# Optimization experiments

Measured on AMD Instinct MI355X. Metric: run time of the kernel, lower is better.

The kernel has to match this reference:

```python
import jax, jax.numpy as jnp
import numpy as np

B, N, C = 8, 1374, 768
H = 12
HD = C // H  # 64
HIDDEN = int(C * 4.0)  # 3072
EPS = 1e-5


def setup_inputs() -> dict:
    key = jax.random.key(0)
    ks = jax.random.split(key, 12)
    s = 0.02
    return {
        "x": jax.random.normal(ks[0], (B, N, C), jnp.float32),
        "rope_freqs": jax.random.normal(ks[1], (1, N, 1, HD), jnp.float32),
        "ln1_g": jnp.ones((C,), jnp.float32),
        "ln1_b": jnp.zeros((C,), jnp.float32),
        "qkv_w": jax.random.normal(ks[2], (3 * C, C), jnp.float32) * s,
        "qkv_b": jnp.zeros((3 * C,), jnp.float32),
        "proj_w": jax.random.normal(ks[3], (C, C), jnp.float32) * s,
        "proj_b": jnp.zeros((C,), jnp.float32),
        "ln2_g": jnp.ones((C,), jnp.float32),
        "ln2_b": jnp.zeros((C,), jnp.float32),
        "w1": jax.random.normal(ks[4], (HIDDEN, C), jnp.float32) * s,
        "b1": jnp.zeros((HIDDEN,), jnp.float32),
        "w2": jax.random.normal(ks[5], (HIDDEN, C), jnp.float32) * s,
        "b2": jnp.zeros((HIDDEN,), jnp.float32),
        "w3": jax.random.normal(ks[6], (C, HIDDEN), jnp.float32) * s,
        "b3": jnp.zeros((C,), jnp.float32),
    }


def _layernorm(x, g, b):
    mu = jnp.mean(x, axis=-1, keepdims=True)
    var = jnp.mean(jnp.square(x - mu), axis=-1, keepdims=True)
    return (x - mu) * jax.lax.rsqrt(var + EPS) * g + b


def _rotate_half(x):
    x1, x2 = jnp.split(x, 2, axis=-1)
    return jnp.concatenate([-x2, x1], axis=-1)


def _apply_rope(q, k, freqs):
    # freqs: [1, N, 1, HD] -> [1, 1, N, HD] (matches torch permute(0,2,1,3))
    f = jnp.transpose(freqs, (0, 2, 1, 3))
    cos, sin = jnp.cos(f), jnp.sin(f)
    q_rot = q * cos + _rotate_half(q) * sin
    k_rot = k * cos + _rotate_half(k) * sin
    return q_rot, k_rot


def reference(x, rope_freqs, ln1_g, ln1_b, qkv_w, qkv_b, proj_w, proj_b,
              ln2_g, ln2_b, w1, b1, w2, b2, w3, b3):
    scale = HD ** -0.5
    # --- Attention branch ---
    h = _layernorm(x, ln1_g, ln1_b)
    qkv = jnp.einsum('bnc,dc->bnd', h, qkv_w) + qkv_b          # [B,N,3C]
    qkv = qkv.reshape(B, N, 3, H, HD).transpose(2, 0, 3, 1, 4)  # [3,B,H,N,HD]
    q, k, v = qkv[0], qkv[1], qkv[2]
    # rope_freqs covers all N tokens -> n_special = 0 path
    q, k = _apply_rope(q, k, rope_freqs)
    attn = jnp.einsum('bhnd,bhmd->bhnm', q, k) * scale          # [B,H,N,N]
    attn = jax.nn.softmax(attn, axis=-1)
    o = jnp.einsum('bhnm,bhmd->bhnd', attn, v)                  # [B,H,N,HD]
    o = o.transpose(0, 2, 1, 3).reshape(B, N, C)
    o = jnp.einsum('bnc,dc->bnd', o, proj_w) + proj_b
    x = x + o
    # --- SwiGLU MLP branch ---
    h2 = _layernorm(x, ln2_g, ln2_b)
    x1 = jnp.einsum('bnc,hc->bnh', h2, w1) + b1
    x2 = jnp.einsum('bnc,hc->bnh', h2, w2) + b2
    hid = jax.nn.silu(x1) * x2
    mlp_out = jnp.einsum('bnh,ch->bnc', hid, w3) + b3
    return x + mlp_out
```

## Files before the change

kernel.cpp:

```cpp
#include <hip/hip_runtime.h>
#include <stdint.h>

#define B_ 8
#define N_ 1374
#define C_ 768
#define H_ 12
#define HD_ 64
#define HID_ 3072
#define M_ (B_*N_)
#define MPAD_ 11008
#define QT_ 22
#define QT2_ 11

#define QSC_ 0.18033688011112042f

typedef __attribute__((ext_vector_type(8))) short short8;
typedef __attribute__((ext_vector_type(4))) float f32x4;
typedef __attribute__((ext_vector_type(4))) _Float16 half4;
typedef __attribute__((ext_vector_type(2))) _Float16 half2v;

__device__ __forceinline__ unsigned short f2bf(float f) {
  unsigned u = __float_as_uint(f);
  u += 0x7FFF + ((u >> 16) & 1);
  return (unsigned short)(u >> 16);
}
__device__ __forceinline__ float bf2f(unsigned short h) {
  return __uint_as_float(((unsigned)h) << 16);
}
__device__ __forceinline__ unsigned short f2h(float f) {
  return __builtin_bit_cast(unsigned short, (_Float16)f);
}

__device__ __forceinline__ half2v pkrtz(float a, float b) {
  return __builtin_bit_cast(half2v, __builtin_amdgcn_cvt_pkrtz(a, b));
}

#if __has_builtin(__builtin_amdgcn_global_load_lds)
#define HAVE_GLL 1
#endif

__device__ __forceinline__ void gld16(const unsigned short* g, unsigned short* l) {
#ifdef HAVE_GLL
  __builtin_amdgcn_global_load_lds((const __attribute__((address_space(1))) void*)g,
                                   (__attribute__((address_space(3))) void*)l, 16, 0, 0);
#else
  *(short8*)l = *(const short8*)g;
#endif
}

__global__ __launch_bounds__(256) void cvt5_kernel(
    const float* __restrict__ s0, const float* __restrict__ s1,
    const float* __restrict__ s2, const float* __restrict__ s3,
    const float* __restrict__ s4, unsigned short* __restrict__ out) {
  int id = blockIdx.x * 256 + threadIdx.x;
  const float* src; int off;
  if (id < 442368)        { src = s0; off = id; }
  else if (id < 589824)   { src = s1; off = id - 442368; }
  else if (id < 1179648)  { src = s2; off = id - 589824; }
  else if (id < 1769472)  { src = s3; off = id - 1179648; }
  else                    { src = s4; off = id - 1769472; }
  float4 v = ((const float4*)src)[off];
  ushort4 o;
  o.x = f2bf(v.x); o.y = f2bf(v.y); o.z = f2bf(v.z); o.w = f2bf(v.w);
  ((ushort4*)out)[id] = o;
}

__global__ __launch_bounds__(256) void ln_kernel(const float* __restrict__ in,
    const float* __restrict__ g, const float* __restrict__ bta,
    unsigned short* __restrict__ out) {
  int row = blockIdx.x;
  int t = threadIdx.x;
  const float* xr = in + (size_t)row * C_;
  float v0 = xr[t], v1 = xr[t + 256], v2 = xr[t + 512];
  float s1 = v0 + v1 + v2;
  float s2 = v0*v0 + v1*v1 + v2*v2;
  for (int off = 1; off < 64; off <<= 1) {
    s1 += __shfl_xor(s1, off, 64);
    s2 += __shfl_xor(s2, off, 64);
  }
  __shared__ float r1[4], r2[4];
  int wave = t >> 6, lane = t & 63;
  if (lane == 0) { r1[wave] = s1; r2[wave] = s2; }
  __syncthreads();
  float tot1 = r1[0] + r1[1] + r1[2] + r1[3];
  float tot2 = r2[0] + r2[1] + r2[2] + r2[3];
  float mu = tot1 * (1.0f / C_);
  float var = tot2 * (1.0f / C_) - mu * mu;
  float rs = rsqrtf(var + 1e-5f);
  size_t ob = (size_t)row * C_;
  out[ob + t]       = f2bf((v0 - mu) * rs * g[t]       + bta[t]);
  out[ob + t + 256] = f2bf((v1 - mu) * rs * g[t + 256] + bta[t + 256]);
  out[ob + t + 512] = f2bf((v2 - mu) * rs * g[t + 512] + bta[t + 512]);
}

template<int EPI, int ROPE, int TM, int SWZ>
__global__ __launch_bounds__(256, (TM == 64) ? 4 : 2) void gemm_bt(
    const unsigned short* __restrict__ A,
    const unsigned short* __restrict__ W,
    void* __restrict__ outp,
    const float* __restrict__ bias0,
    const float* __restrict__ resid,
    const float* __restrict__ freqs,
    int K, int ldo, int Mvalid, int X)
{
  constexpr int MI = TM / 32;
  __shared__ __align__(16) unsigned short As[2][TM * 32];
  __shared__ __align__(16) unsigned short Bs[2][4096];
  const int t = threadIdx.x;
  const int lane = t & 63;
  const int wave = t >> 6;
  const int wm = (wave >> 1) * (TM / 2);
  const int wn = (wave & 1) * 64;
  const int lr = lane & 15;
  const int lg = lane >> 4;
  const int lk = lg * 8;
  int bx, by;
  if (SWZ) {
    int Y = gridDim.x / X;
    int lin = blockIdx.x;
    int sgsz = X * 8;
    int sg = lin / sgsz;
    int base_y = sg * 8;
    int rows = Y - base_y; if (rows > 8) rows = 8;
    int within = lin - sg * sgsz;
    by = base_y + within % rows;
    bx = within / rows;
  } else {
    bx = blockIdx.x % X;
    by = blockIdx.x / X;
  }
  const int tm0 = by * TM;
  const int tn0 = bx * 128;
  const int r0 = t >> 2;
  const int c0 = (t & 3) * 8;
  const unsigned short* ga0 = A + (size_t)(tm0 + r0) * K + c0;
  const unsigned short* ga1 = A + (size_t)(tm0 + 64 + r0) * K + c0;
  const unsigned short* gb0 = W + (size_t)(tn0 + r0) * K + c0;
  const unsigned short* gb1 = W + (size_t)(tn0 + 64 + r0) * K + c0;
  f32x4 zero = {0.f, 0.f, 0.f, 0.f};
  f32x4 acc[MI][4];
#pragma unroll
  for (int mi = 0; mi < MI; ++mi)
#pragma unroll
    for (int ni = 0; ni < 4; ++ni) acc[mi][ni] = zero;

  for (int kt = 0; kt < K; kt += 64) {
    __syncthreads();
    gld16(ga0 + kt,      &As[0][t * 8]);
    gld16(ga0 + kt + 32, &As[1][t * 8]);
    if (TM == 128) {
      gld16(ga1 + kt,      &As[0][2048 + t * 8]);
      gld16(ga1 + kt + 32, &As[1][2048 + t * 8]);
    }
    gld16(gb0 + kt,      &Bs[0][t * 8]);
    gld16(gb1 + kt,      &Bs[0][2048 + t * 8]);
    gld16(gb0 + kt + 32, &Bs[1][t * 8]);
    gld16(gb1 + kt + 32, &Bs[1][2048 + t * 8]);
    __syncthreads();
#pragma unroll
    for (int u = 0; u < 2; ++u) {
      short8 af[MI], bfr[4];
#pragma unroll
      for (int mi = 0; mi < MI; ++mi) af[mi] = *(const short8*)&As[u][(wm + mi * 16 + lr) * 32 + lk];
#pragma unroll
      for (int ni = 0; ni < 4; ++ni) bfr[ni] = *(const short8*)&Bs[u][(wn + ni * 16 + lr) * 32 + lk];
#pragma unroll
      for (int mi = 0; mi < MI; ++mi)
#pragma unroll
        for (int ni = 0; ni < 4; ++ni)
          acc[mi][ni] = __builtin_amdgcn_mfma_f32_16x16x32_bf16(af[mi], bfr[ni], acc[mi][ni], 0, 0, 0);
    }
  }

  if (EPI == 0) {
    bool dorope = ROPE && ((tn0 + wn) < 1536);
    bool isq    = ROPE && ((tn0 + wn) < 768);
    bool isv    = ROPE && ((tn0 + wn) >= 1536);
#pragma unroll
    for (int mi = 0; mi < MI; ++mi) {
#pragma unroll
      for (int p = 0; p < 2; ++p) {
        int col1 = tn0 + wn + p * 16 + lr;
        int col2 = col1 + 32;
        float bv1 = bias0[col1], bv2 = bias0[col2];
        int e = p * 16 + lr;
#pragma unroll
        for (int r = 0; r < 4; ++r) {
          int row = tm0 + wm + mi * 16 + lg * 4 + r;
          float v1 = acc[mi][p][r] + bv1;
          float v2 = acc[mi][p + 2][r] + bv2;
          float o1 = v1, o2 = v2;
          if (dorope) {
            int n = row % N_;
            float f1 = freqs[n * HD_ + e];
            float f2 = freqs[n * HD_ + e + 32];
            float c1, s1, c2, s2;
            __sincosf(f1, &s1, &c1);
            __sincosf(f2, &s2, &c2);
            o1 = v1 * c1 - v2 * s1;
            o2 = v2 * c2 + v1 * s2;
          }
          if (isq) { o1 *= QSC_; o2 *= QSC_; }
          size_t base = (size_t)row * ldo;
          if (isv) {
            ((unsigned short*)outp)[base + col1] = f2h(o1);
            ((unsigned short*)outp)[base + col2] = f2h(o2);
          } else {
            ((unsigned short*)outp)[base + col1] = f2bf(o1);
            ((unsigned short*)outp)[base + col2] = f2bf(o2);
          }
        }
      }
    }
  } else {
#pragma unroll
    for (int mi = 0; mi < MI; ++mi) {
#pragma unroll
      for (int ni = 0; ni < 4; ++ni) {
        int col = tn0 + wn + ni * 16 + lr;
        float bval = bias0[col];
#pragma unroll
        for (int r = 0; r < 4; ++r) {
          int row = tm0 + wm + mi * 16 + lg * 4 + r;
          float v = acc[mi][ni][r] + bval;
          size_t idx = (size_t)row * ldo + col;
          if (EPI == 1) {
            if (row < Mvalid) ((float*)outp)[idx] = resid[idx] + v;
          } else {
            if (row < Mvalid) ((float*)outp)[idx] = ((float*)outp)[idx] + v;
          }
        }
      }
    }
  }
}

__global__ __launch_bounds__(256, 2) void gemm_w12_swiglu(
    const unsigned short* __restrict__ A,
    const unsigned short* __restrict__ W1,
    const unsigned short* __restrict__ W2,
    unsigned short* __restrict__ hid,
    const float* __restrict__ b1,
    const float* __restrict__ b2)
{
  __shared__ __align__(16) unsigned short As[2][4096];
  __shared__ __align__(16) unsigned short B1s[2][2048];
  __shared__ __align__(16) unsigned short B2s[2][2048];
  const int t = threadIdx.x;
  const int lane = t & 63;
  const int wave = t >> 6;
  const int wm = (wave >> 1) * 64;
  const int wn = (wave & 1) * 32;
  const int lr = lane & 15;
  const int lg = lane >> 4;
  const int lk = lg * 8;
  const int tm0 = blockIdx.y * 128;
  const int tn0 = blockIdx.x * 64;
  const int r0 = t >> 2;
  const int c0 = (t & 3) * 8;
  const unsigned short* ga0 = A + (size_t)(tm0 + r0) * 768 + c0;
  const unsigned short* ga1 = A + (size_t)(tm0 + 64 + r0) * 768 + c0;
  const unsigned short* g1 = W1 + (size_t)(tn0 + r0) * 768 + c0;
  const unsigned short* g2 = W2 + (size_t)(tn0 + r0) * 768 + c0;
  f32x4 zero = {0.f, 0.f, 0.f, 0.f};
  f32x4 acc1[4][2], acc2[4][2];
#pragma unroll
  for (int mi = 0; mi < 4; ++mi)
#pragma unroll
    for (int ni = 0; ni < 2; ++ni) { acc1[mi][ni] = zero; acc2[mi][ni] = zero; }

  for (int kt = 0; kt < 768; kt += 64) {
    __syncthreads();
    gld16(ga0 + kt,      &As[0][t * 8]);
    gld16(ga1 + kt,      &As[0][2048 + t * 8]);
    gld16(ga0 + kt + 32, &As[1][t * 8]);
    gld16(ga1 + kt + 32, &As[1][2048 + t * 8]);
    gld16(g1 + kt,       &B1s[0][t * 8]);
    gld16(g1 + kt + 32,  &B1s[1][t * 8]);
    gld16(g2 + kt,       &B2s[0][t * 8]);
    gld16(g2 + kt + 32,  &B2s[1][t * 8]);
    __syncthreads();
#pragma unroll
    for (int u = 0; u < 2; ++u) {
      short8 af[4], b1f[2], b2f[2];
#pragma unroll
      for (int mi = 0; mi < 4; ++mi) af[mi] = *(const short8*)&As[u][(wm + mi * 16 + lr) * 32 + lk];
#pragma unroll
      for (int ni = 0; ni < 2; ++ni) {
        b1f[ni] = *(const short8*)&B1s[u][(wn + ni * 16 + lr) * 32 + lk];
        b2f[ni] = *(const short8*)&B2s[u][(wn + ni * 16 + lr) * 32 + lk];
      }
#pragma unroll
      for (int mi = 0; mi < 4; ++mi)
#pragma unroll
        for (int ni = 0; ni < 2; ++ni) {
          acc1[mi][ni] = __builtin_amdgcn_mfma_f32_16x16x32_bf16(af[mi], b1f[ni], acc1[mi][ni], 0, 0, 0);
          acc2[mi][ni] = __builtin_amdgcn_mfma_f32_16x16x32_bf16(af[mi], b2f[ni], acc2[mi][ni], 0, 0, 0);
        }
    }
  }
#pragma unroll
  for (int mi = 0; mi < 4; ++mi) {
#pragma unroll
    for (int ni = 0; ni < 2; ++ni) {
      int col = tn0 + wn + ni * 16 + lr;
      float bv1 = b1[col], bv2 = b2[col];
#pragma unroll
      for (int r = 0; r < 4; ++r) {
        int row = tm0 + wm + mi * 16 + lg * 4 + r;
        float a1 = acc1[mi][ni][r] + bv1;
        float a2 = acc2[mi][ni][r] + bv2;
        float h = a1 / (1.f + __expf(-a1)) * a2;
        hid[(size_t)row * HID_ + col] = f2bf(h);
      }
    }
  }
}

struct FalseT { static constexpr bool value = false; };
struct TrueT  { static constexpr bool value = true;  };

__global__ __launch_bounds__(256, 4) void attn_kernel(
    const unsigned short* __restrict__ qkv,
    unsigned short* __restrict__ o2)
{
  __shared__ __align__(16) unsigned short Ks[2][64 * 80];
  __shared__ __align__(16) _Float16 Vt[2][64 * 72];
  int bidx = blockIdx.x;
  int qt = bidx % QT2_;
  int bh = bidx / QT2_;
  int head = bh % H_;
  int b = bh / H_;
  int t = threadIdx.x, lane = t & 63, wave = t >> 6;
  int lr = lane & 15, lg = lane >> 4;

  short8 bq[2][2];
#pragma unroll
  for (int s = 0; s < 2; ++s) {
    int m = qt * 128 + wave * 32 + s * 16 + lr;
    int mc = (m < N_) ? m : (N_ - 1);
    const unsigned short* qrow = qkv + (size_t)(b * N_ + mc) * 2304 + head * HD_;
    bq[s][0] = *(const short8*)(qrow + lg * 8);
    bq[s][1] = *(const short8*)(qrow + 32 + lg * 8);
  }

  f32x4 zero = {0.f, 0.f, 0.f, 0.f};
  f32x4 acc[2][4];
  f32x4 dacc[2];
#pragma unroll
  for (int s = 0; s < 2; ++s) {
    dacc[s] = zero;
#pragma unroll
    for (int dt = 0; dt < 4; ++dt) acc[s][dt] = zero;
  }

  const int kr0 = t >> 3;
  const int kc  = (t & 7) * 8;
  const int vp  = t & 31;
  const int vc  = t >> 5;
  const unsigned short* kbase = qkv + (size_t)(b * N_) * 2304 + 768  + head * HD_ + kc;
  const unsigned short* vbase = qkv + (size_t)(b * N_) * 2304 + 1536 + head * HD_ + vc * 8;

  short8 krg[2], vrg[2];
  auto issue = [&](int jt) {
    int j0 = jt * 64 + kr0;        if (j0 >= N_) j0 = N_ - 1;
    int j1 = jt * 64 + kr0 + 32;   if (j1 >= N_) j1 = N_ - 1;
    int vj0 = jt * 64 + 2 * vp;    if (vj0 >= N_) vj0 = N_ - 1;
    int vj1 = jt * 64 + 2 * vp + 1; if (vj1 >= N_) vj1 = N_ - 1;
    krg[0] = *(const short8*)(kbase + (size_t)j0 * 2304);
    krg[1] = *(const short8*)(kbase + (size_t)j1 * 2304);
    vrg[0] = *(const short8*)(vbase + (size_t)vj0 * 2304);
    vrg[1] = *(const short8*)(vbase + (size_t)vj1 * 2304);
  };

  const half4 vones = {(_Float16)1.f, (_Float16)1.f, (_Float16)1.f, (_Float16)1.f};

  auto compute = [&](int jt, const unsigned short* ksb, const _Float16* vtb, auto tailc) {
    constexpr bool TAIL = decltype(tailc)::value;
#pragma unroll
    for (int st = 0; st < 4; ++st) {
      short8 ak0 = *(const short8*)&ksb[(st * 16 + lr) * 80 + lg * 8];
      short8 ak1 = *(const short8*)&ksb[(st * 16 + lr) * 80 + 32 + lg * 8];
      int jb = jt * 64 + st * 16 + lg * 4;
      half4 pf[2];
#pragma unroll
      for (int s = 0; s < 2; ++s) {
        f32x4 sc = zero;
        sc = __builtin_amdgcn_mfma_f32_16x16x32_bf16(ak0, bq[s][0], sc, 0, 0, 0);
        sc = __builtin_amdgcn_mfma_f32_16x16x32_bf16(ak1, bq[s][1], sc, 0, 0, 0);
        float p[4];
#pragma unroll
        for (int r = 0; r < 4; ++r) {
          float pv = exp2f(sc[r]);
          if (TAIL) pv = (jb + r < N_) ? pv : 0.f;
          p[r] = pv;
        }
        union { half4 v; half2v h[2]; } pu;
        pu.h[0] = pkrtz(p[0], p[1]);
        pu.h[1] = pkrtz(p[2], p[3]);
        pf[s] = pu.v;
      }
      dacc[0] = __builtin_amdgcn_mfma_f32_16x16x16f16(pf[0], vones, dacc[0], 0, 0, 0);
      dacc[1] = __builtin_amdgcn_mfma_f32_16x16x16f16(pf[1], vones, dacc[1], 0, 0, 0);
#pragma unroll
      for (int dt = 0; dt < 4; ++dt) {
        half4 bv = *(const half4*)&vtb[(dt * 16 + lr) * 72 + st * 16 + lg * 4];
        acc[0][dt] = __builtin_amdgcn_mfma_f32_16x16x16f16(pf[0], bv, acc[0][dt], 0, 0, 0);
        acc[1][dt] = __builtin_amdgcn_mfma_f32_16x16x16f16(pf[1], bv, acc[1][dt], 0, 0, 0);
      }
    }
  };

  issue(0);
  int cur = 0;
  for (int jt = 0; jt < QT_; ++jt) {
    unsigned short* ksb = &Ks[cur][0];
    _Float16* vtb = &Vt[cur][0];
    *(short8*)&ksb[kr0 * 80 + kc] = krg[0];
    *(short8*)&ksb[(kr0 + 32) * 80 + kc] = krg[1];
#pragma unroll
    for (int i = 0; i < 8; ++i) {
      unsigned lo = (unsigned short)vrg[0][i];
      unsigned hi = (unsigned short)vrg[1][i];
      *(unsigned*)&Vt[cur][(vc * 8 + i) * 72 + 2 * vp] = lo | (hi << 16);
    }
    __syncthreads();
    issue(jt + 1);
    if (jt == QT_ - 1) compute(jt, ksb, vtb, TrueT{});
    else               compute(jt, ksb, vtb, FalseT{});
    cur ^= 1;
  }

#pragma unroll
  for (int s = 0; s < 2; ++s) {
#pragma unroll
    for (int r = 0; r < 4; ++r) {
      float dm = dacc[s][r];
      int m = qt * 128 + wave * 32 + s * 16 + lg * 4 + r;
      if (m < N_) {
        float invd = 1.f / dm;
        unsigned short* orow = o2 + (size_t)(b * N_ + m) * C_ + head * HD_;
#pragma unroll
        for (int dt = 0; dt < 4; ++dt)
          orow[dt * 16 + lr] = f2bf(acc[s][dt][r] * invd);
      }
    }
  }
}

extern "C" void kernel_launch(void* const* d_in, const int* in_sizes, int n_in,
                              void* d_out, int out_size, void* d_ws, size_t ws_size,
                              hipStream_t stream) {
  const float* x      = (const float*)d_in[0];
  const float* freqs  = (const float*)d_in[1];
  const float* ln1_g  = (const float*)d_in[2];
  const float* ln1_b  = (const float*)d_in[3];
  const float* qkv_w  = (const float*)d_in[4];
  const float* qkv_b  = (const float*)d_in[5];
  const float* proj_w = (const float*)d_in[6];
  const float* proj_b = (const float*)d_in[7];
  const float* ln2_g  = (const float*)d_in[8];
  const float* ln2_b  = (const float*)d_in[9];
  const float* w1     = (const float*)d_in[10];
  const float* b1     = (const float*)d_in[11];
  const float* w2     = (const float*)d_in[12];
  const float* b2     = (const float*)d_in[13];
  const float* w3     = (const float*)d_in[14];
  const float* b3     = (const float*)d_in[15];
  float* out = (float*)d_out;
  char* ws = (char*)d_ws;

  unsigned short* hB     = (unsigned short*)(ws + 0);
  unsigned short* wqkvB  = (unsigned short*)(ws + 16908288);
  unsigned short* wprojB = (unsigned short*)(ws + 20447232);
  unsigned short* w12B   = (unsigned short*)(ws + 21626880);
  unsigned short* w3B    = (unsigned short*)(ws + 31064064);
  unsigned short* qkvB   = (unsigned short*)(ws + 35782656);
  unsigned short* o2B    = (unsigned short*)(ws + 86507520);
  unsigned short* hidB   = qkvB;

  cvt5_kernel<<<9216, 256, 0, stream>>>(qkv_w, proj_w, w1, w2, w3, wqkvB);

  ln_kernel<<<M_, 256, 0, stream>>>(x, ln1_g, ln1_b, hB);
  gemm_bt<0, 1, 128, 1><<<18 * 86, 256, 0, stream>>>(hB, wqkvB, qkvB, qkv_b, nullptr, freqs, 768, 2304, M_, 18);
  attn_kernel<<<B_ * H_ * QT2_, 256, 0, stream>>>(qkvB, o2B);
  gemm_bt<1, 0, 64, 1><<<6 * 172, 256, 0, stream>>>(o2B, wprojB, out, proj_b, x, nullptr, 768, 768, M_, 6);

  ln_kernel<<<M_, 256, 0, stream>>>(out, ln2_g, ln2_b, hB);
  gemm_w12_swiglu<<<dim3(48, 86), 256, 0, stream>>>(hB, w12B, w12B + 3072 * 768, hidB, b1, b2);
  gemm_bt<3, 0, 64, 1><<<6 * 172, 256, 0, stream>>>(hidB, w3B, out, b3, nullptr, nullptr, 3072, 768, M_, 6);
}
```

Before: 531.6 us.

## Switch attention to 32x32 MFMA tiles and enlarge w3 GEMM row tile

Attention now uses 32x32x16 bf16 MFMA for QK^T and 32x32x8 f16 MFMA for PV and the row-sum. Each wave covers 32 query rows with one tile instead of two 16-row tiles, which cuts LDS fragment reloads and the MFMA instruction count. The K LDS row stride goes from 80 to 88 to change the bank mapping for the new read pattern, and launch bounds drop to 3 blocks per SIMD to allow more registers for the 16-wide accumulators. Separately, the final w3 GEMM switches to a 128-row tile with half the blocks, trading parallelism for more reuse per block.

```diff
diff --git a/kernel.cpp b/kernel.cpp
--- a/kernel.cpp
+++ b/kernel.cpp
@@ -16,6 +16,7 @@
 
 typedef __attribute__((ext_vector_type(8))) short short8;
 typedef __attribute__((ext_vector_type(4))) float f32x4;
+typedef __attribute__((ext_vector_type(16))) float f32x16;
 typedef __attribute__((ext_vector_type(4))) _Float16 half4;
 typedef __attribute__((ext_vector_type(2))) _Float16 half2v;
 
@@ -320,11 +321,11 @@
 struct FalseT { static constexpr bool value = false; };
 struct TrueT  { static constexpr bool value = true;  };
 
-__global__ __launch_bounds__(256, 4) void attn_kernel(
+__global__ __launch_bounds__(256, 3) void attn_kernel(
     const unsigned short* __restrict__ qkv,
     unsigned short* __restrict__ o2)
 {
-  __shared__ __align__(16) unsigned short Ks[2][64 * 80];
+  __shared__ __align__(16) unsigned short Ks[2][64 * 88];
   __shared__ __align__(16) _Float16 Vt[2][64 * 72];
   int bidx = blockIdx.x;
   int qt = bidx % QT2_;
@@ -332,27 +333,21 @@
   int head = bh % H_;
   int b = bh / H_;
   int t = threadIdx.x, lane = t & 63, wave = t >> 6;
-  int lr = lane & 15, lg = lane >> 4;
-
-  short8 bq[2][2];
-#pragma unroll
-  for (int s = 0; s < 2; ++s) {
-    int m = qt * 128 + wave * 32 + s * 16 + lr;
+  int lq = lane & 31, lg2 = lane >> 5;
+
+  short8 bq[4];
+  {
+    int m = qt * 128 + wave * 32 + lq;
     int mc = (m < N_) ? m : (N_ - 1);
     const unsigned short* qrow = qkv + (size_t)(b * N_ + mc) * 2304 + head * HD_;
-    bq[s][0] = *(const short8*)(qrow + lg * 8);
-    bq[s][1] = *(const short8*)(qrow + 32 + lg * 8);
-  }
-
-  f32x4 zero = {0.f, 0.f, 0.f, 0.f};
-  f32x4 acc[2][4];
-  f32x4 dacc[2];
-#pragma unroll
-  for (int s = 0; s < 2; ++s) {
-    dacc[s] = zero;
-#pragma unroll
-    for (int dt = 0; dt < 4; ++dt) acc[s][dt] = zero;
-  }
+#pragma unroll
+    for (int c = 0; c < 4; ++c)
+      bq[c] = *(const short8*)(qrow + c * 16 + lg2 * 8);
+  }
+
+  f32x16 acc[2];
+  f32x16 dacc;
+  acc[0] = {}; acc[1] = {}; dacc = {};
 
   const int kr0 = t >> 3;
   const int kc  = (t & 7) * 8;
@@ -378,35 +373,47 @@
   auto compute = [&](int jt, const unsigned short* ksb, const _Float16* vtb, auto tailc) {
     constexpr bool TAIL = decltype(tailc)::value;
 #pragma unroll
-    for (int st = 0; st < 4; ++st) {
-      short8 ak0 = *(const short8*)&ksb[(st * 16 + lr) * 80 + lg * 8];
-      short8 ak1 = *(const short8*)&ksb[(st * 16 + lr) * 80 + 32 + lg * 8];
-      int jb = jt * 64 + st * 16 + lg * 4;
-      half4 pf[2];
-#pragma unroll
-      for (int s = 0; s < 2; ++s) {
-        f32x4 sc = zero;
-        sc = __builtin_amdgcn_mfma_f32_16x16x32_bf16(ak0, bq[s][0], sc, 0, 0, 0);
-        sc = __builtin_amdgcn_mfma_f32_16x16x32_bf16(ak1, bq[s][1], sc, 0, 0, 0);
-        float p[4];
-#pragma unroll
-        for (int r = 0; r < 4; ++r) {
-          float pv = exp2f(sc[r]);
-          if (TAIL) pv = (jb + r < N_) ? pv : 0.f;
-          p[r] = pv;
+    for (int st2 = 0; st2 < 2; ++st2) {
+      f32x16 sc = {};
+      {
+        const unsigned short* krow = &ksb[(st2 * 32 + lq) * 88 + lg2 * 8];
+        short8 ak0 = *(const short8*)(krow);
+        short8 ak1 = *(const short8*)(krow + 16);
+        short8 ak2 = *(const short8*)(krow + 32);
+        short8 ak3 = *(const short8*)(krow + 48);
+        sc = __builtin_amdgcn_mfma_f32_32x32x16_bf16(ak0, bq[0], sc, 0, 0, 0);
+        sc = __builtin_amdgcn_mfma_f32_32x32x16_bf16(ak1, bq[1], sc, 0, 0, 0);
+        sc = __builtin_amdgcn_mfma_f32_32x32x16_bf16(ak2, bq[2], sc, 0, 0, 0);
+        sc = __builtin_amdgcn_mfma_f32_32x32x16_bf16(ak3, bq[3], sc, 0, 0, 0);
+      }
+#pragma unroll
+      for (int r = 0; r < 16; ++r) {
+        float pv = exp2f(sc[r]);
+        if (TAIL) {
+          int jw = (r & 3) + 8 * (r >> 2) + 4 * lg2;
+          int j = jt * 64 + st2 * 32 + jw;
+          pv = (j < N_) ? pv : 0.f;
         }
+        sc[r] = pv;
+      }
+      half4 pf[4];
+#pragma unroll
+      for (int ks = 0; ks < 4; ++ks) {
         union { half4 v; half2v h[2]; } pu;
-        pu.h[0] = pkrtz(p[0], p[1]);
-        pu.h[1] = pkrtz(p[2], p[3]);
-        pf[s] = pu.v;
-      }
-      dacc[0] = __builtin_amdgcn_mfma_f32_16x16x16f16(pf[0], vones, dacc[0], 0, 0, 0);
-      dacc[1] = __builtin_amdgcn_mfma_f32_16x16x16f16(pf[1], vones, dacc[1], 0, 0, 0);
-#pragma unroll
-      for (int dt = 0; dt < 4; ++dt) {
-        half4 bv = *(const half4*)&vtb[(dt * 16 + lr) * 72 + st * 16 + lg * 4];
-        acc[0][dt] = __builtin_amdgcn_mfma_f32_16x16x16f16(pf[0], bv, acc[0][dt], 0, 0, 0);
-        acc[1][dt] = __builtin_amdgcn_mfma_f32_16x16x16f16(pf[1], bv, acc[1][dt], 0, 0, 0);
+        pu.h[0] = pkrtz(sc[ks * 4 + 0], sc[ks * 4 + 1]);
+        pu.h[1] = pkrtz(sc[ks * 4 + 2], sc[ks * 4 + 3]);
+        pf[ks] = pu.v;
+      }
+#pragma unroll
+      for (int ks = 0; ks < 4; ++ks)
+        dacc = __builtin_amdgcn_mfma_f32_32x32x8f16(pf[ks], vones, dacc, 0, 0, 0);
+#pragma unroll
+      for (int dt = 0; dt < 2; ++dt) {
+#pragma unroll
+        for (int ks = 0; ks < 4; ++ks) {
+          half4 bv = *(const half4*)&vtb[(dt * 32 + lq) * 72 + st2 * 32 + ks * 8 + lg2 * 4];
+          acc[dt] = __builtin_amdgcn_mfma_f32_32x32x8f16(pf[ks], bv, acc[dt], 0, 0, 0);
+        }
       }
     }
   };
@@ -416,8 +423,8 @@
   for (int jt = 0; jt < QT_; ++jt) {
     unsigned short* ksb = &Ks[cur][0];
     _Float16* vtb = &Vt[cur][0];
-    *(short8*)&ksb[kr0 * 80 + kc] = krg[0];
-    *(short8*)&ksb[(kr0 + 32) * 80 + kc] = krg[1];
+    *(short8*)&ksb[kr0 * 88 + kc] = krg[0];
+    *(short8*)&ksb[(kr0 + 32) * 88 + kc] = krg[1];
 #pragma unroll
     for (int i = 0; i < 8; ++i) {
       unsigned lo = (unsigned short)vrg[0][i];
@@ -432,18 +439,14 @@
   }
 
 #pragma unroll
-  for (int s = 0; s < 2; ++s) {
-#pragma unroll
-    for (int r = 0; r < 4; ++r) {
-      float dm = dacc[s][r];
-      int m = qt * 128 + wave * 32 + s * 16 + lg * 4 + r;
-      if (m < N_) {
-        float invd = 1.f / dm;
-        unsigned short* orow = o2 + (size_t)(b * N_ + m) * C_ + head * HD_;
-#pragma unroll
-        for (int dt = 0; dt < 4; ++dt)
-          orow[dt * 16 + lr] = f2bf(acc[s][dt][r] * invd);
-      }
+  for (int r = 0; r < 16; ++r) {
+    int qw = (r & 3) + 8 * (r >> 2) + 4 * lg2;
+    int m = qt * 128 + wave * 32 + qw;
+    if (m < N_) {
+      float invd = 1.f / dacc[r];
+      unsigned short* orow = o2 + (size_t)(b * N_ + m) * C_ + head * HD_ + lq;
+      orow[0]  = f2bf(acc[0][r] * invd);
+      orow[32] = f2bf(acc[1][r] * invd);
     }
   }
 }
@@ -488,5 +491,5 @@
 
   ln_kernel<<<M_, 256, 0, stream>>>(out, ln2_g, ln2_b, hB);
   gemm_w12_swiglu<<<dim3(48, 86), 256, 0, stream>>>(hB, w12B, w12B + 3072 * 768, hidB, b1, b2);
-  gemm_bt<3, 0, 64, 1><<<6 * 172, 256, 0, stream>>>(hidB, w3B, out, b3, nullptr, nullptr, 3072, 768, M_, 6);
-}
+  gemm_bt<3, 0, 128, 1><<<6 * 86, 256, 0, stream>>>(hidB, w3B, out, b3, nullptr, nullptr, 3072, 768, M_, 6);
+}
```

Result: no change. 534.5 us (+0.6%).
